# Optimization experiments

Measured on AMD Instinct MI355X. Metric: run time of the kernel, lower is better.

## Reference

```python
import jax, jax.numpy as jnp
import numpy as np
from math import log2

N_QUBITS = 11
N_LAYERS = 2
DEGREE = 3
N_TIMESTEPS = 8
BSZ = 64
DIM = 2 ** N_QUBITS
N_ROTS = 4 * N_QUBITS * N_LAYERS  # 88


def _ry(theta):
    # batched RY(theta): (B,) -> (B,2,2) complex64
    h = 0.5 * theta
    c, s = jnp.cos(h), jnp.sin(h)
    U = jnp.stack([jnp.stack([c, -s], -1), jnp.stack([s, c], -1)], -2)
    return U.astype(jnp.complex64)


def _rx(theta):
    # batched RX(theta): (B,) -> (B,2,2) complex64
    h = 0.5 * theta
    c = jnp.cos(h).astype(jnp.complex64)
    s = (-1j) * jnp.sin(h).astype(jnp.complex64)
    return jnp.stack([jnp.stack([c, s], -1), jnp.stack([s, c], -1)], -2)


def _apply_1q(state, U, w):
    # state: (B,) + (2,)*n ; apply per-batch 2x2 U on wire w
    s = jnp.moveaxis(state, w + 1, 1)
    shp = s.shape
    s = s.reshape(shp[0], 2, -1)
    s = jnp.einsum('bij,bjr->bir', U, s)
    return jnp.moveaxis(s.reshape(shp), 1, w + 1)


def _apply_crx(state, theta, c_w, t_w):
    # controlled-RX: apply RX on target wire t_w where control wire c_w is |1>
    U = _rx(theta)
    s = jnp.moveaxis(state, (c_w + 1, t_w + 1), (1, 2))
    shp = s.shape
    s = s.reshape(shp[0], 2, 2, -1)
    s1 = jnp.einsum('bij,bjr->bir', U, s[:, 1])
    s = jnp.concatenate([s[:, :1], s1[:, None]], axis=1).reshape(shp)
    return jnp.moveaxis(s, (1, 2), (c_w + 1, t_w + 1))


def _sim14_evolve(state, params):
    # faithful sim14_circuit (v3 fixed RY-CRX gate set), batched angles
    n = state.ndim - 1
    layers = params.shape[1] // (4 * n)
    idx = 0
    for _ in range(layers):
        for i in range(n):
            state = _apply_1q(state, _ry(params[:, idx]), i); idx += 1
        for i in range(n - 1, -1, -1):
            state = _apply_crx(state, params[:, idx], i, (i + 1) % n); idx += 1
        for i in range(n):
            state = _apply_1q(state, _ry(params[:, idx]), i); idx += 1
        for i in [n - 1] + list(range(n - 1)):
            state = _apply_crx(state, params[:, idx], i, (i - 1) % n); idx += 1
    return state


def _apply_unitaries(base, uparams, coeffs):
    # apply_unitaries_pl: repeat_interleave + evolve + LCU einsum
    bsz, T, n_rots = uparams.shape
    dim = base.shape[1]
    n = int(round(log2(dim)))
    flat = uparams.reshape(bsz * T, n_rots)
    rep = jnp.repeat(base, T, axis=0).reshape((bsz * T,) + (2,) * n)
    ev = _sim14_evolve(rep, flat).reshape(bsz, T, dim)
    return jnp.einsum('bti,bt->bi', ev, coeffs.astype(jnp.complex64))


def setup_inputs() -> dict:
    key = jax.random.key(0)
    k1, k2, k3, k4 = jax.random.split(key, 4)
    base_states = jax.random.normal(k1, (BSZ, DIM), dtype=jnp.float32)
    unitary_params = jax.random.normal(k2, (BSZ, N_TIMESTEPS, N_ROTS), dtype=jnp.float32)
    lcu_coeffs = jax.random.normal(k3, (BSZ, N_TIMESTEPS), dtype=jnp.float32)
    poly_coeffs = jax.random.normal(k4, (DEGREE + 1,), dtype=jnp.float32)
    return {"base_states": base_states, "unitary_params": unitary_params,
            "lcu_coeffs": lcu_coeffs, "poly_coeffs": poly_coeffs}


def reference(base_states, unitary_params, lcu_coeffs, poly_coeffs):
    # evaluate_polynomial_state_pl (QSVT polynomial state preparation)
    base = base_states.astype(jnp.complex64)
    base = base / jnp.linalg.norm(base, axis=1, keepdims=True)  # valid quantum state
    pc = poly_coeffs.astype(jnp.complex64)
    acc = pc[0] * base
    working = base
    for k in range(1, poly_coeffs.shape[0]):
        working = _apply_unitaries(working, unitary_params, lcu_coeffs)
        acc = acc + pc[k] * working
    out = acc / jnp.sum(jnp.abs(poly_coeffs)).astype(jnp.complex64)
    # return real/imag stacked so output is real-valued: (bsz, dim, 2)
    return jnp.stack([out.real, out.imag], axis=-1)
```

## Files before the change

### kernel.cpp

```cpp
#include <hip/hip_runtime.h>
#include <utility>

#define DIM 2048
#define NQ 11
#define NROT 88
#define BSZ 64
#define NT 8
#define NPC 4

constexpr int g_type(int G) {
    int j = G % 44;
    return (j < 11 || (j >= 22 && j < 33)) ? 0 : 1;
}
constexpr int g_pt(int G) {
    int j = G % 44;
    if (j < 11) return 10 - j;
    if (j < 22) { int i = 21 - j; int tw = (i + 1 == NQ) ? 0 : i + 1; return 10 - tw; }
    if (j < 33) return 10 - (j - 22);
    if (j == 33) return 1;
    int i = j - 34; int tw = (i + 10) % NQ; return 10 - tw;
}
constexpr int g_pcb(int G) {
    int j = G % 44;
    if (j >= 11 && j < 22) { int i = 21 - j; return 10 - i; }
    if (j == 33) return 0;
    if (j >= 34) { int i = j - 34; return 10 - i; }
    return -1;
}
constexpr int block_parity(int G) {
    int c = 0;
    for (int g = 0; g < G; ++g) if (g_pt(g) >= 8) c ^= 1;
    return c;
}

template<int LB>
__device__ __forceinline__ float lx(float x) {
    if constexpr (LB == 0) {
        return __int_as_float(__builtin_amdgcn_update_dpp(
            __float_as_int(x), __float_as_int(x), 0xB1, 0xF, 0xF, true));
    } else if constexpr (LB == 1) {
        return __int_as_float(__builtin_amdgcn_update_dpp(
            __float_as_int(x), __float_as_int(x), 0x4E, 0xF, 0xF, true));
    } else if constexpr (LB == 2) {
        return __int_as_float(__builtin_amdgcn_ds_swizzle(__float_as_int(x), 0x101F));
    } else if constexpr (LB == 3) {
        return __int_as_float(__builtin_amdgcn_ds_swizzle(__float_as_int(x), 0x201F));
    } else if constexpr (LB == 4) {
        return __int_as_float(__builtin_amdgcn_ds_swizzle(__float_as_int(x), 0x401F));
    } else {
        return __shfl_xor(x, 32, 64);
    }
}

template<int G>
__device__ __forceinline__ void apply_gate(
    float2 (&R)[2], float2 (&I)[2],
    const float* __restrict__ sc, const float* __restrict__ ss,
    float4* __restrict__ exbuf, const int tid)
{
    constexpr int type = g_type(G);
    constexpr int pt   = g_pt(G);
    constexpr int pcb  = g_pcb(G);
    const float c = sc[G];
    const float s = ss[G];

    if constexpr (pt == 0) {
        if constexpr (type == 0) {
#pragma unroll
            for (int m = 0; m < 2; ++m) {
                float er = R[m].x, orr = R[m].y, ei = I[m].x, oi = I[m].y;
                R[m].x = c*er - s*orr;  R[m].y = s*er + c*orr;
                I[m].x = c*ei - s*oi;   I[m].y = s*ei + c*oi;
            }
        } else if constexpr (pcb == 1) {
            float er = R[1].x, orr = R[1].y, ei = I[1].x, oi = I[1].y;
            R[1].x = c*er + s*oi;   I[1].x = c*ei - s*orr;
            R[1].y = c*orr + s*ei;  I[1].y = c*oi - s*er;
        } else {
            const bool ctrl = (tid >> (pcb - 2)) & 1;
            if (ctrl) {
#pragma unroll
                for (int m = 0; m < 2; ++m) {
                    float er = R[m].x, orr = R[m].y, ei = I[m].x, oi = I[m].y;
                    R[m].x = c*er + s*oi;   I[m].x = c*ei - s*orr;
                    R[m].y = c*orr + s*ei;  I[m].y = c*oi - s*er;
                }
            }
        }
    } else if constexpr (pt == 1) {
        if constexpr (type == 0) {
            float2 l = R[0], h = R[1], li = I[0], hi = I[1];
            R[0].x = c*l.x - s*h.x;   R[0].y = c*l.y - s*h.y;
            R[1].x = s*l.x + c*h.x;   R[1].y = s*l.y + c*h.y;
            I[0].x = c*li.x - s*hi.x; I[0].y = c*li.y - s*hi.y;
            I[1].x = s*li.x + c*hi.x; I[1].y = s*li.y + c*hi.y;
        } else if constexpr (pcb == 0) {
            float lr = R[0].y, li = I[0].y, hr = R[1].y, hi = I[1].y;
            R[0].y = c*lr + s*hi;   I[0].y = c*li - s*hr;
            R[1].y = c*hr + s*li;   I[1].y = c*hi - s*lr;
        } else {
            const bool ctrl = (tid >> (pcb - 2)) & 1;
            if (ctrl) {
                float2 l = R[0], h = R[1], li = I[0], hi = I[1];
                R[0].x = c*l.x + s*hi.x;  R[0].y = c*l.y + s*hi.y;
                I[0].x = c*li.x - s*h.x;  I[0].y = c*li.y - s*h.y;
                R[1].x = c*h.x + s*li.x;  R[1].y = c*h.y + s*li.y;
                I[1].x = c*hi.x - s*l.x;  I[1].y = c*hi.y - s*l.y;
            }
        }
    } else if constexpr (pt <= 7) {
        constexpr int lb = pt - 2;
        if constexpr (type == 0) {
            const float sg = ((tid >> lb) & 1) ? s : -s;
#pragma unroll
            for (int m = 0; m < 2; ++m) {
                float prx = lx<lb>(R[m].x), pry = lx<lb>(R[m].y);
                float pix = lx<lb>(I[m].x), piy = lx<lb>(I[m].y);
                R[m].x = c*R[m].x + sg*prx;  R[m].y = c*R[m].y + sg*pry;
                I[m].x = c*I[m].x + sg*pix;  I[m].y = c*I[m].y + sg*piy;
            }
        } else if constexpr (pcb == 0) {
#pragma unroll
            for (int m = 0; m < 2; ++m) {
                float pry = lx<lb>(R[m].y), piy = lx<lb>(I[m].y);
                R[m].y = c*R[m].y + s*piy;
                I[m].y = c*I[m].y - s*pry;
            }
        } else if constexpr (pcb == 1) {
            float prx = lx<lb>(R[1].x), pry = lx<lb>(R[1].y);
            float pix = lx<lb>(I[1].x), piy = lx<lb>(I[1].y);
            R[1].x = c*R[1].x + s*pix;  R[1].y = c*R[1].y + s*piy;
            I[1].x = c*I[1].x - s*prx;  I[1].y = c*I[1].y - s*pry;
        } else {
            const bool ctrl = (tid >> (pcb - 2)) & 1;
            if (ctrl) {
#pragma unroll
                for (int m = 0; m < 2; ++m) {
                    float prx = lx<lb>(R[m].x), pry = lx<lb>(R[m].y);
                    float pix = lx<lb>(I[m].x), piy = lx<lb>(I[m].y);
                    R[m].x = c*R[m].x + s*pix;  R[m].y = c*R[m].y + s*piy;
                    I[m].x = c*I[m].x - s*prx;  I[m].y = c*I[m].y - s*pry;
                }
            }
        }
    } else {
        constexpr int par = block_parity(G);
        float4* buf = exbuf + par * 1024;
        const int ptid = tid ^ (1 << (pt - 2));
        if constexpr (type == 0) {
#pragma unroll
            for (int m = 0; m < 2; ++m)
                buf[m * 512 + tid] = make_float4(R[m].x, R[m].y, I[m].x, I[m].y);
            __syncthreads();
            const float sg = ((tid >> (pt - 2)) & 1) ? s : -s;
#pragma unroll
            for (int m = 0; m < 2; ++m) {
                float4 v = buf[m * 512 + ptid];
                R[m].x = c*R[m].x + sg*v.x;  R[m].y = c*R[m].y + sg*v.y;
                I[m].x = c*I[m].x + sg*v.z;  I[m].y = c*I[m].y + sg*v.w;
            }
        } else if constexpr (pcb == 0) {
            float2* f2 = (float2*)buf;
#pragma unroll
            for (int m = 0; m < 2; ++m)
                f2[m * 512 + tid] = make_float2(R[m].y, I[m].y);
            __syncthreads();
#pragma unroll
            for (int m = 0; m < 2; ++m) {
                float2 v = f2[m * 512 + ptid];
                R[m].y = c*R[m].y + s*v.y;
                I[m].y = c*I[m].y - s*v.x;
            }
        } else if constexpr (pcb == 1) {
            buf[tid] = make_float4(R[1].x, R[1].y, I[1].x, I[1].y);
            __syncthreads();
            float4 v = buf[ptid];
            R[1].x = c*R[1].x + s*v.z;  R[1].y = c*R[1].y + s*v.w;
            I[1].x = c*I[1].x - s*v.x;  I[1].y = c*I[1].y - s*v.y;
        } else {
            const bool ctrl = (tid >> (pcb - 2)) & 1;
            if (ctrl) {
#pragma unroll
                for (int m = 0; m < 2; ++m)
                    buf[m * 512 + tid] = make_float4(R[m].x, R[m].y, I[m].x, I[m].y);
            }
            __syncthreads();
            if (ctrl) {
#pragma unroll
                for (int m = 0; m < 2; ++m) {
                    float4 v = buf[m * 512 + ptid];
                    R[m].x = c*R[m].x + s*v.z;  R[m].y = c*R[m].y + s*v.w;
                    I[m].x = c*I[m].x - s*v.x;  I[m].y = c*I[m].y - s*v.y;
                }
            }
        }
    }
}

template<int... Gs>
__device__ __forceinline__ void apply_all(std::integer_sequence<int, Gs...>,
    float2 (&R)[2], float2 (&I)[2],
    const float* __restrict__ sc, const float* __restrict__ ss,
    float4* __restrict__ exbuf, const int tid)
{
    (apply_gate<Gs>(R, I, sc, ss, exbuf, tid), ...);
}

template<int MODE>
__global__ __launch_bounds__(512) void evolve_kernel(
    const void* __restrict__ src, const float* __restrict__ uparams,
    const float* __restrict__ lcu, float2* __restrict__ pout,
    const float* __restrict__ pcoef, float2* __restrict__ acc, int kprev)
{
    __shared__ float4 exbuf[2048];
    __shared__ float sc[NROT], ss[NROT];
    __shared__ float red[9];

    const int b = blockIdx.x >> 3;
    const int t = blockIdx.x & 7;
    const int tid = threadIdx.x;

    float2 R[2], I[2];
    if constexpr (MODE == 0) {
        const float4* b4 = (const float4*)((const float*)src + (size_t)b * DIM);
        float4 v = b4[tid];
        float loc = v.x*v.x + v.y*v.y + v.z*v.z + v.w*v.w;
        for (int off = 32; off > 0; off >>= 1) loc += __shfl_down(loc, off, 64);
        if ((tid & 63) == 0) red[tid >> 6] = loc;
        __syncthreads();
        if (tid == 0) { float sm = 0.f; for (int w = 0; w < 8; ++w) sm += red[w]; red[8] = sm; }
        __syncthreads();
        const float inv = rsqrtf(red[8]);
        R[0] = make_float2(v.x * inv, v.y * inv);
        R[1] = make_float2(v.z * inv, v.w * inv);
        I[0] = make_float2(0.f, 0.f);
        I[1] = make_float2(0.f, 0.f);
        if (t == 0) {
            const float p0 = pcoef[0];
            float4* a4 = (float4*)(acc + (size_t)b * DIM);
            a4[tid*2+0] = make_float4(p0*R[0].x, 0.f, p0*R[0].y, 0.f);
            a4[tid*2+1] = make_float4(p0*R[1].x, 0.f, p0*R[1].y, 0.f);
        }
    } else if constexpr (MODE == 1) {
        R[0] = R[1] = I[0] = I[1] = make_float2(0.f, 0.f);
        const float2* s2 = (const float2*)src;
        for (int cc = 0; cc < NT; ++cc) {
            const float4* p4 = (const float4*)(s2 + ((size_t)b * NT + cc) * DIM);
#pragma unroll
            for (int m = 0; m < 2; ++m) {
                float4 v = p4[tid*2+m];
                R[m].x += v.x; I[m].x += v.y; R[m].y += v.z; I[m].y += v.w;
            }
        }
        if (t == 0) {
            const float pk = pcoef[kprev];
            float4* a4 = (float4*)(acc + (size_t)b * DIM);
#pragma unroll
            for (int m = 0; m < 2; ++m) {
                float4 v = a4[tid*2+m];
                v.x += pk * R[m].x; v.y += pk * I[m].x;
                v.z += pk * R[m].y; v.w += pk * I[m].y;
                a4[tid*2+m] = v;
            }
        }
    } else {
        const float2* s2 = (const float2*)src;
        const float4* p4 = (const float4*)(s2 + (size_t)b * DIM);
#pragma unroll
        for (int m = 0; m < 2; ++m) {
            float4 v = p4[tid*2+m];
            R[m].x = v.x; I[m].x = v.y; R[m].y = v.z; I[m].y = v.w;
        }
    }

    if (tid < NROT) {
        float th = 0.5f * uparams[(b * NT + t) * NROT + tid];
        sc[tid] = cosf(th); ss[tid] = sinf(th);
    }
    __syncthreads();

    apply_all(std::make_integer_sequence<int, NROT>{}, R, I, sc, ss, exbuf, tid);

    const float coeff = lcu[b * NT + t];
    float4* o4 = (float4*)(pout + ((size_t)b * NT + t) * DIM);
#pragma unroll
    for (int m = 0; m < 2; ++m)
        o4[tid*2+m] = make_float4(coeff*R[m].x, coeff*I[m].x, coeff*R[m].y, coeff*I[m].y);
}

__global__ __launch_bounds__(256) void final_kernel(
    const float2* __restrict__ partial, const float* __restrict__ pcoef,
    const float2* __restrict__ acc, float* __restrict__ out)
{
    int b = blockIdx.x >> 3;
    int i = ((blockIdx.x & 7) << 8) | threadIdx.x;
    float sr = 0.f, si = 0.f;
    for (int c = 0; c < NT; ++c) {
        float2 v = partial[((size_t)b * NT + c) * DIM + i];
        sr += v.x; si += v.y;
    }
    float sabs = 0.f;
    for (int q = 0; q < NPC; ++q) sabs += fabsf(pcoef[q]);
    float invn = 1.0f / sabs;
    float pk = pcoef[NPC - 1];
    float2 a = acc[(size_t)b * DIM + i];
    out[((size_t)b * DIM + i) * 2 + 0] = (a.x + pk * sr) * invn;
    out[((size_t)b * DIM + i) * 2 + 1] = (a.y + pk * si) * invn;
}

__global__ __launch_bounds__(256) void setup_kernel(
    const float* __restrict__ base, const float* __restrict__ pc,
    float2* __restrict__ working, float2* __restrict__ acc)
{
    int b = blockIdx.x;
    int tid = threadIdx.x;
    __shared__ float red[4];
    float ssum = 0.f;
    for (int i = tid; i < DIM; i += 256) {
        float v = base[b * DIM + i];
        ssum += v * v;
    }
    for (int off = 32; off > 0; off >>= 1) ssum += __shfl_down(ssum, off, 64);
    if ((tid & 63) == 0) red[tid >> 6] = ssum;
    __syncthreads();
    if (tid == 0) red[0] = red[0] + red[1] + red[2] + red[3];
    __syncthreads();
    float inv = rsqrtf(red[0]);
    float p0 = pc[0];
    for (int i = tid; i < DIM; i += 256) {
        float v = base[b * DIM + i] * inv;
        working[b * DIM + i] = make_float2(v, 0.f);
        acc[b * DIM + i] = make_float2(p0 * v, 0.f);
    }
}

__global__ __launch_bounds__(256) void reduce_kernel(
    const float2* __restrict__ partial, const float* __restrict__ pcoef,
    float2* __restrict__ working, float2* __restrict__ acc,
    float* __restrict__ out, int k, int last)
{
    int b = blockIdx.x >> 3;
    int i = ((blockIdx.x & 7) << 8) | threadIdx.x;
    float pk = pcoef[k];
    float sr = 0.f, si = 0.f;
    for (int c = 0; c < NT; ++c) {
        float2 v = partial[((size_t)b * NT + c) * DIM + i];
        sr += v.x; si += v.y;
    }
    working[b * DIM + i] = make_float2(sr, si);
    float2 a = acc[b * DIM + i];
    a.x += pk * sr; a.y += pk * si;
    acc[b * DIM + i] = a;
    if (last) {
        float sabs = 0.f;
        for (int q = 0; q < NPC; ++q) sabs += fabsf(pcoef[q]);
        float invn = 1.0f / sabs;
        out[((size_t)b * DIM + i) * 2 + 0] = a.x * invn;
        out[((size_t)b * DIM + i) * 2 + 1] = a.y * invn;
    }
}

extern "C" void kernel_launch(void* const* d_in, const int* in_sizes, int n_in,
                              void* d_out, int out_size, void* d_ws, size_t ws_size,
                              hipStream_t stream) {
    const float* base = (const float*)d_in[0];
    const float* upar = (const float*)d_in[1];
    const float* lcu  = (const float*)d_in[2];
    const float* pc   = (const float*)d_in[3];
    float* out = (float*)d_out;

    const size_t plane = (size_t)BSZ * DIM * sizeof(float2);
    char* ws = (char*)d_ws;

    if (ws_size >= (1 + 3 * (size_t)NT) * plane) {
        float2* acc = (float2*)ws;
        float2* pA  = (float2*)(ws + plane);
        float2* pB  = (float2*)(ws + plane + (size_t)NT * plane);
        float2* pC  = (float2*)(ws + plane + (size_t)2 * NT * plane);
        evolve_kernel<0><<<BSZ * NT, 512, 0, stream>>>(base, upar, lcu, pA, pc, acc, 0);
        evolve_kernel<1><<<BSZ * NT, 512, 0, stream>>>(pA,   upar, lcu, pB, pc, acc, 1);
        evolve_kernel<1><<<BSZ * NT, 512, 0, stream>>>(pB,   upar, lcu, pC, pc, acc, 2);
        final_kernel<<<BSZ * 8, 256, 0, stream>>>(pC, pc, acc, out);
    } else {
        float2* working = (float2*)ws;
        float2* acc     = (float2*)(ws + plane);
        float2* pA      = (float2*)(ws + 2 * plane);
        setup_kernel<<<BSZ, 256, 0, stream>>>(base, pc, working, acc);
        for (int k = 1; k <= NPC - 1; ++k) {
            evolve_kernel<2><<<BSZ * NT, 512, 0, stream>>>(working, upar, lcu, pA, pc, acc, 0);
            reduce_kernel<<<BSZ * 8, 256, 0, stream>>>(pA, pc, working, acc, out,
                                                       k, (k == NPC - 1) ? 1 : 0);
        }
    }
}
```

Before: 87.17 us.

## Precompute rotation cos/sin table and use permlane swaps for cross-row exchanges

Adds a prep kernel that computes cos/sin for every rotation angle once into a workspace table. The evolve kernels now read angles from global memory instead of computing them per block, which removes a shared-memory fill and a barrier. Exchanges across 16- and 32-lane distances now use permlane16/32 swap intrinsics through a sum-based algebraic rewrite (k1=c-sg), and the 8-lane exchange uses DPP instead of ds_swizzle. It also raises launch bounds to 4 blocks per CU, at the cost of one extra kernel launch and a different rounding pattern in the sum formulation.

Result: slower. 96.55 us (+10.8%).

```diff
diff --git a/kernel.cpp b/kernel.cpp
--- a/kernel.cpp
+++ b/kernel.cpp
@@ -7,6 +7,18 @@
 #define BSZ 64
 #define NT 8
 #define NPC 4
+#define NANG (BSZ * NT * NROT)
+
+#if __has_builtin(__builtin_amdgcn_permlane16_swap)
+#define HAVE_PL16 1
+#else
+#define HAVE_PL16 0
+#endif
+#if __has_builtin(__builtin_amdgcn_permlane32_swap)
+#define HAVE_PL32 1
+#else
+#define HAVE_PL32 0
+#endif
 
 constexpr int g_type(int G) {
     int j = G % 44;
@@ -32,9 +44,12 @@
     for (int g = 0; g < G; ++g) if (g_pt(g) >= 8) c ^= 1;
     return c;
 }
+constexpr bool use_sum_tier(int lb) {
+    return (lb == 4 && HAVE_PL16) || (lb == 5 && HAVE_PL32);
+}
 
 template<int LB>
-__device__ __forceinline__ float lx(float x) {
+__device__ __forceinline__ float lxp(float x) {
     if constexpr (LB == 0) {
         return __int_as_float(__builtin_amdgcn_update_dpp(
             __float_as_int(x), __float_as_int(x), 0xB1, 0xF, 0xF, true));
@@ -44,7 +59,8 @@
     } else if constexpr (LB == 2) {
         return __int_as_float(__builtin_amdgcn_ds_swizzle(__float_as_int(x), 0x101F));
     } else if constexpr (LB == 3) {
-        return __int_as_float(__builtin_amdgcn_ds_swizzle(__float_as_int(x), 0x201F));
+        return __int_as_float(__builtin_amdgcn_update_dpp(
+            __float_as_int(x), __float_as_int(x), 0x128, 0xF, 0xF, true));
     } else if constexpr (LB == 4) {
         return __int_as_float(__builtin_amdgcn_ds_swizzle(__float_as_int(x), 0x401F));
     } else {
@@ -52,17 +68,36 @@
     }
 }
 
+template<int LB>
+__device__ __forceinline__ float lxsum(float x) {
+#if HAVE_PL16
+    if constexpr (LB == 4) {
+        unsigned u = __float_as_uint(x);
+        auto r = __builtin_amdgcn_permlane16_swap(u, u, false, false);
+        return __uint_as_float(r[0]) + __uint_as_float(r[1]);
+    }
+#endif
+#if HAVE_PL32
+    if constexpr (LB == 5) {
+        unsigned u = __float_as_uint(x);
+        auto r = __builtin_amdgcn_permlane32_swap(u, u, false, false);
+        return __uint_as_float(r[0]) + __uint_as_float(r[1]);
+    }
+#endif
+    return x + lxp<LB>(x);
+}
+
 template<int G>
 __device__ __forceinline__ void apply_gate(
     float2 (&R)[2], float2 (&I)[2],
-    const float* __restrict__ sc, const float* __restrict__ ss,
+    const float* __restrict__ cs,
     float4* __restrict__ exbuf, const int tid)
 {
     constexpr int type = g_type(G);
     constexpr int pt   = g_pt(G);
     constexpr int pcb  = g_pcb(G);
-    const float c = sc[G];
-    const float s = ss[G];
+    const float c = cs[2*G];
+    const float s = cs[2*G+1];
 
     if constexpr (pt == 0) {
         if constexpr (type == 0) {
@@ -110,36 +145,76 @@
         }
     } else if constexpr (pt <= 7) {
         constexpr int lb = pt - 2;
-        if constexpr (type == 0) {
-            const float sg = ((tid >> lb) & 1) ? s : -s;
-#pragma unroll
-            for (int m = 0; m < 2; ++m) {
-                float prx = lx<lb>(R[m].x), pry = lx<lb>(R[m].y);
-                float pix = lx<lb>(I[m].x), piy = lx<lb>(I[m].y);
-                R[m].x = c*R[m].x + sg*prx;  R[m].y = c*R[m].y + sg*pry;
-                I[m].x = c*I[m].x + sg*pix;  I[m].y = c*I[m].y + sg*piy;
-            }
-        } else if constexpr (pcb == 0) {
-#pragma unroll
-            for (int m = 0; m < 2; ++m) {
-                float pry = lx<lb>(R[m].y), piy = lx<lb>(I[m].y);
-                R[m].y = c*R[m].y + s*piy;
-                I[m].y = c*I[m].y - s*pry;
-            }
-        } else if constexpr (pcb == 1) {
-            float prx = lx<lb>(R[1].x), pry = lx<lb>(R[1].y);
-            float pix = lx<lb>(I[1].x), piy = lx<lb>(I[1].y);
-            R[1].x = c*R[1].x + s*pix;  R[1].y = c*R[1].y + s*piy;
-            I[1].x = c*I[1].x - s*prx;  I[1].y = c*I[1].y - s*pry;
+        if constexpr (use_sum_tier(lb)) {
+            if constexpr (type == 0) {
+                const float sg = ((tid >> lb) & 1) ? s : -s;
+                const float k1 = c - sg;
+#pragma unroll
+                for (int m = 0; m < 2; ++m) {
+                    float srx = lxsum<lb>(R[m].x), sry = lxsum<lb>(R[m].y);
+                    float six = lxsum<lb>(I[m].x), siy = lxsum<lb>(I[m].y);
+                    R[m].x = k1*R[m].x + sg*srx;  R[m].y = k1*R[m].y + sg*sry;
+                    I[m].x = k1*I[m].x + sg*six;  I[m].y = k1*I[m].y + sg*siy;
+                }
+            } else if constexpr (pcb == 0) {
+#pragma unroll
+                for (int m = 0; m < 2; ++m) {
+                    float sR = lxsum<lb>(R[m].y), sI = lxsum<lb>(I[m].y);
+                    float r = R[m].y, i = I[m].y;
+                    R[m].y = c*r - s*i + s*sI;
+                    I[m].y = c*i + s*r - s*sR;
+                }
+            } else if constexpr (pcb == 1) {
+                float sRx = lxsum<lb>(R[1].x), sRy = lxsum<lb>(R[1].y);
+                float sIx = lxsum<lb>(I[1].x), sIy = lxsum<lb>(I[1].y);
+                float rx = R[1].x, ry = R[1].y, ix = I[1].x, iy = I[1].y;
+                R[1].x = c*rx - s*ix + s*sIx;  R[1].y = c*ry - s*iy + s*sIy;
+                I[1].x = c*ix + s*rx - s*sRx;  I[1].y = c*iy + s*ry - s*sRy;
+            } else {
+                const bool ctrl = (tid >> (pcb - 2)) & 1;
+                if (ctrl) {
+#pragma unroll
+                    for (int m = 0; m < 2; ++m) {
+                        float sRx = lxsum<lb>(R[m].x), sRy = lxsum<lb>(R[m].y);
+                        float sIx = lxsum<lb>(I[m].x), sIy = lxsum<lb>(I[m].y);
+                        float rx = R[m].x, ry = R[m].y, ix = I[m].x, iy = I[m].y;
+                        R[m].x = c*rx - s*ix + s*sIx;  R[m].y = c*ry - s*iy + s*sIy;
+                        I[m].x = c*ix + s*rx - s*sRx;  I[m].y = c*iy + s*ry - s*sRy;
+                    }
+                }
+            }
         } else {
-            const bool ctrl = (tid >> (pcb - 2)) & 1;
-            if (ctrl) {
-#pragma unroll
-                for (int m = 0; m < 2; ++m) {
-                    float prx = lx<lb>(R[m].x), pry = lx<lb>(R[m].y);
-                    float pix = lx<lb>(I[m].x), piy = lx<lb>(I[m].y);
-                    R[m].x = c*R[m].x + s*pix;  R[m].y = c*R[m].y + s*piy;
-                    I[m].x = c*I[m].x - s*prx;  I[m].y = c*I[m].y - s*pry;
+            if constexpr (type == 0) {
+                const float sg = ((tid >> lb) & 1) ? s : -s;
+#pragma unroll
+                for (int m = 0; m < 2; ++m) {
+                    float prx = lxp<lb>(R[m].x), pry = lxp<lb>(R[m].y);
+                    float pix = lxp<lb>(I[m].x), piy = lxp<lb>(I[m].y);
+                    R[m].x = c*R[m].x + sg*prx;  R[m].y = c*R[m].y + sg*pry;
+                    I[m].x = c*I[m].x + sg*pix;  I[m].y = c*I[m].y + sg*piy;
+                }
+            } else if constexpr (pcb == 0) {
+#pragma unroll
+                for (int m = 0; m < 2; ++m) {
+                    float pry = lxp<lb>(R[m].y), piy = lxp<lb>(I[m].y);
+                    R[m].y = c*R[m].y + s*piy;
+                    I[m].y = c*I[m].y - s*pry;
+                }
+            } else if constexpr (pcb == 1) {
+                float prx = lxp<lb>(R[1].x), pry = lxp<lb>(R[1].y);
+                float pix = lxp<lb>(I[1].x), piy = lxp<lb>(I[1].y);
+                R[1].x = c*R[1].x + s*pix;  R[1].y = c*R[1].y + s*piy;
+                I[1].x = c*I[1].x - s*prx;  I[1].y = c*I[1].y - s*pry;
+            } else {
+                const bool ctrl = (tid >> (pcb - 2)) & 1;
+                if (ctrl) {
+#pragma unroll
+                    for (int m = 0; m < 2; ++m) {
+                        float prx = lxp<lb>(R[m].x), pry = lxp<lb>(R[m].y);
+                        float pix = lxp<lb>(I[m].x), piy = lxp<lb>(I[m].y);
+                        R[m].x = c*R[m].x + s*pix;  R[m].y = c*R[m].y + s*piy;
+                        I[m].x = c*I[m].x - s*prx;  I[m].y = c*I[m].y - s*pry;
+                    }
                 }
             }
         }
@@ -200,25 +275,36 @@
 template<int... Gs>
 __device__ __forceinline__ void apply_all(std::integer_sequence<int, Gs...>,
     float2 (&R)[2], float2 (&I)[2],
-    const float* __restrict__ sc, const float* __restrict__ ss,
+    const float* __restrict__ cs,
     float4* __restrict__ exbuf, const int tid)
 {
-    (apply_gate<Gs>(R, I, sc, ss, exbuf, tid), ...);
+    (apply_gate<Gs>(R, I, cs, exbuf, tid), ...);
+}
+
+__global__ __launch_bounds__(256) void prep_kernel(
+    const float* __restrict__ upar, float* __restrict__ cs)
+{
+    int i = blockIdx.x * 256 + threadIdx.x;
+    if (i < NANG) {
+        float th = 0.5f * upar[i];
+        cs[2*i]   = cosf(th);
+        cs[2*i+1] = sinf(th);
+    }
 }
 
 template<int MODE>
-__global__ __launch_bounds__(512) void evolve_kernel(
-    const void* __restrict__ src, const float* __restrict__ uparams,
+__global__ __launch_bounds__(512, 4) void evolve_kernel(
+    const void* __restrict__ src, const float* __restrict__ cs_table,
     const float* __restrict__ lcu, float2* __restrict__ pout,
     const float* __restrict__ pcoef, float2* __restrict__ acc, int kprev)
 {
     __shared__ float4 exbuf[2048];
-    __shared__ float sc[NROT], ss[NROT];
     __shared__ float red[9];
 
     const int b = blockIdx.x >> 3;
     const int t = blockIdx.x & 7;
     const int tid = threadIdx.x;
+    const float* __restrict__ cs = cs_table + (size_t)(b * NT + t) * (2 * NROT);
 
     float2 R[2], I[2];
     if constexpr (MODE == 0) {
@@ -273,13 +359,7 @@
         }
     }
 
-    if (tid < NROT) {
-        float th = 0.5f * uparams[(b * NT + t) * NROT + tid];
-        sc[tid] = cosf(th); ss[tid] = sinf(th);
-    }
-    __syncthreads();
-
-    apply_all(std::make_integer_sequence<int, NROT>{}, R, I, sc, ss, exbuf, tid);
+    apply_all(std::make_integer_sequence<int, NROT>{}, R, I, cs, exbuf, tid);
 
     const float coeff = lcu[b * NT + t];
     float4* o4 = (float4*)(pout + ((size_t)b * NT + t) * DIM);
@@ -370,24 +450,30 @@
     float* out = (float*)d_out;
 
     const size_t plane = (size_t)BSZ * DIM * sizeof(float2);
+    const size_t cs_bytes = 512 * 1024;
     char* ws = (char*)d_ws;
-
-    if (ws_size >= (1 + 3 * (size_t)NT) * plane) {
-        float2* acc = (float2*)ws;
-        float2* pA  = (float2*)(ws + plane);
-        float2* pB  = (float2*)(ws + plane + (size_t)NT * plane);
-        float2* pC  = (float2*)(ws + plane + (size_t)2 * NT * plane);
-        evolve_kernel<0><<<BSZ * NT, 512, 0, stream>>>(base, upar, lcu, pA, pc, acc, 0);
-        evolve_kernel<1><<<BSZ * NT, 512, 0, stream>>>(pA,   upar, lcu, pB, pc, acc, 1);
-        evolve_kernel<1><<<BSZ * NT, 512, 0, stream>>>(pB,   upar, lcu, pC, pc, acc, 2);
+    float* cs = (float*)ws;
+
+    const int prep_blocks = (NANG + 255) / 256;
+
+    if (ws_size >= cs_bytes + (1 + 3 * (size_t)NT) * plane) {
+        float2* acc = (float2*)(ws + cs_bytes);
+        float2* pA  = (float2*)(ws + cs_bytes + plane);
+        float2* pB  = (float2*)(ws + cs_bytes + plane + (size_t)NT * plane);
+        float2* pC  = (float2*)(ws + cs_bytes + plane + (size_t)2 * NT * plane);
+        prep_kernel<<<prep_blocks, 256, 0, stream>>>(upar, cs);
+        evolve_kernel<0><<<BSZ * NT, 512, 0, stream>>>(base, cs, lcu, pA, pc, acc, 0);
+        evolve_kernel<1><<<BSZ * NT, 512, 0, stream>>>(pA,   cs, lcu, pB, pc, acc, 1);
+        evolve_kernel<1><<<BSZ * NT, 512, 0, stream>>>(pB,   cs, lcu, pC, pc, acc, 2);
         final_kernel<<<BSZ * 8, 256, 0, stream>>>(pC, pc, acc, out);
     } else {
-        float2* working = (float2*)ws;
-        float2* acc     = (float2*)(ws + plane);
-        float2* pA      = (float2*)(ws + 2 * plane);
+        float2* working = (float2*)(ws + cs_bytes);
+        float2* acc     = (float2*)(ws + cs_bytes + plane);
+        float2* pA      = (float2*)(ws + cs_bytes + 2 * plane);
+        prep_kernel<<<prep_blocks, 256, 0, stream>>>(upar, cs);
         setup_kernel<<<BSZ, 256, 0, stream>>>(base, pc, working, acc);
         for (int k = 1; k <= NPC - 1; ++k) {
-            evolve_kernel<2><<<BSZ * NT, 512, 0, stream>>>(working, upar, lcu, pA, pc, acc, 0);
+            evolve_kernel<2><<<BSZ * NT, 512, 0, stream>>>(working, cs, lcu, pA, pc, acc, 0);
             reduce_kernel<<<BSZ * 8, 256, 0, stream>>>(pA, pc, working, acc, out,
                                                        k, (k == NPC - 1) ? 1 : 0);
         }
```
